# Performance work log

Measured on AMD Instinct MI355X. Metric: run time of the kernel, lower is better.

## Reference

```python
import jax, jax.numpy as jnp
import numpy as np

N_QUBITS = 10
LAYERS = 4


def _ry(theta):
    c = jnp.cos(theta / 2).astype(jnp.complex64)
    s = jnp.sin(theta / 2).astype(jnp.complex64)
    return jnp.array([[c, -s], [s, c]], dtype=jnp.complex64)


def _rot(phi, theta, omega):
    # Rot = RZ(omega) RY(theta) RZ(phi)  (PennyLane convention)
    c = jnp.cos(theta / 2)
    s = jnp.sin(theta / 2)
    e_mm = jnp.exp(-0.5j * (phi + omega))
    e_pm = jnp.exp(0.5j * (phi - omega))
    e_mp = jnp.exp(-0.5j * (phi - omega))
    e_pp = jnp.exp(0.5j * (phi + omega))
    return jnp.array([[e_mm * c, -e_pm * s], [e_mp * s, e_pp * c]], dtype=jnp.complex64)


def _apply_1q(state, U, q):
    # state: (2,)*n complex; contract qubit axis q with 2x2 gate
    s = jnp.tensordot(U, state, axes=[[1], [q]])
    return jnp.moveaxis(s, 0, q)


def _apply_cnot(state, c, t):
    s = jnp.moveaxis(state, (c, t), (0, 1))
    s = jnp.stack([s[0], s[1, ::-1]], axis=0)
    return jnp.moveaxis(s, (0, 1), (c, t))


def _circuit(angles, weights):
    # angles: (n_qubits,) float32, weights: (layers, n_qubits, 3) float32
    n = N_QUBITS
    state = jnp.zeros((2 ** n,), dtype=jnp.complex64).at[0].set(1.0).reshape((2,) * n)
    for q in range(n):  # RY angle embedding
        state = _apply_1q(state, _ry(angles[q]), q)
    for l in range(LAYERS):  # strongly-entangling layers
        for q in range(n):
            state = _apply_1q(state, _rot(weights[l, q, 0], weights[l, q, 1], weights[l, q, 2]), q)
        for q in range(n):  # CNOT ring
            state = _apply_cnot(state, q, (q + 1) % n)
    probs = state.real ** 2 + state.imag ** 2  # (2,)*n
    zexp = []
    for q in range(n):
        p = probs.sum(axis=tuple(a for a in range(n) if a != q))
        zexp.append(p[0] - p[1])
    return jnp.stack(zexp)  # (n_qubits,)


def setup_inputs() -> dict:
    key = jax.random.key(0)
    ks = jax.random.split(key, 6)
    B, D = 8192, 784
    return {
        "x": jax.random.normal(ks[0], (B, D), dtype=jnp.float32),
        "Wp": jax.random.normal(ks[1], (N_QUBITS, D), dtype=jnp.float32) * (1.0 / np.sqrt(D)),
        "bp": jax.random.normal(ks[2], (N_QUBITS,), dtype=jnp.float32) * 0.01,
        "q_weights": jax.random.normal(ks[3], (LAYERS, N_QUBITS, 3), dtype=jnp.float32) * 0.01,
        "Wo": jax.random.normal(ks[4], (10, N_QUBITS), dtype=jnp.float32) * (1.0 / np.sqrt(N_QUBITS)),
        "bo": jax.random.normal(ks[5], (10,), dtype=jnp.float32) * 0.01,
    }


def reference(x, Wp, bp, q_weights, Wo, bo):
    # input projection + tanh
    h = jnp.tanh(x @ Wp.T + bp)  # (B, n_qubits)
    # batched quantum circuit (vmapped statevector simulation)
    q_out = jax.vmap(_circuit, in_axes=(0, None))(h, q_weights)  # (B, n_qubits)
    return q_out @ Wo.T + bo  # (B, 10) logits
```

## Files before the change

kernel.cpp:

```cpp
#include <hip/hip_runtime.h>

#define NQ      10
#define NLAYERS 4
#define D_IN    784
#define BLOCK   256


typedef __attribute__((ext_vector_type(2))) float f2;

__device__ __forceinline__ f2 cswapneg(f2 v) {
    f2 r; r.x = -v.y; r.y = v.x; return r;
}

template<int LB>
__device__ __forceinline__ float lane_xor(float v) {
    if constexpr (LB == 1) {
        return __int_as_float(__builtin_amdgcn_update_dpp(
            0, __float_as_int(v), 0xB1, 0xF, 0xF, false));
    } else if constexpr (LB == 2) {
        return __int_as_float(__builtin_amdgcn_update_dpp(
            0, __float_as_int(v), 0x4E, 0xF, 0xF, false));
    } else {
        return __shfl_xor(v, LB, 64);
    }
}

template<int LB>
__device__ __forceinline__ f2 lane_xor2(f2 v) {
    f2 r; r.x = lane_xor<LB>(v.x); r.y = lane_xor<LB>(v.y); return r;
}

template<int HALF>
__device__ __forceinline__ void plswap(f2 &d, f2 &s) {
    if constexpr (HALF == 32) {
        auto rx = __builtin_amdgcn_permlane32_swap(__float_as_int(d.x), __float_as_int(s.x), false, false);
        auto ry = __builtin_amdgcn_permlane32_swap(__float_as_int(d.y), __float_as_int(s.y), false, false);
        d.x = __int_as_float(rx[0]); s.x = __int_as_float(rx[1]);
        d.y = __int_as_float(ry[0]); s.y = __int_as_float(ry[1]);
    } else {
        auto rx = __builtin_amdgcn_permlane16_swap(__float_as_int(d.x), __float_as_int(s.x), false, false);
        auto ry = __builtin_amdgcn_permlane16_swap(__float_as_int(d.y), __float_as_int(s.y), false, false);
        d.x = __int_as_float(rx[0]); s.x = __int_as_float(rx[1]);
        d.y = __int_as_float(ry[0]); s.y = __int_as_float(ry[1]);
    }
}

template<int HALF>
__device__ __forceinline__ void rot_gate_pl(f2 (&a)[16], float4 gA, float4 gB) {
#pragma unroll
    for (int r = 0; r < 16; r += 2) {
        f2 u = a[r], v = a[r + 1];
        plswap<HALF>(u, v);
        f2 iu = cswapneg(u), iv = cswapneg(v);
        f2 nu = gA.x * u + gA.y * iu + gA.z * v + gA.w * iv;
        f2 nv = gB.x * u + gB.y * iu + gB.z * v + gB.w * iv;
        plswap<HALF>(nu, nv);
        a[r] = nu; a[r + 1] = nv;
    }
}

__device__ __forceinline__ void rot9_fused_pl(f2 (&a)[16], int lane, float4 gA, float4 gB) {
    const bool hi = (lane & 32) != 0;
    const float cux = hi ? gA.z : gA.x, cuy = hi ? gA.w : gA.y;
    const float cvx = hi ? gA.x : gA.z, cvy = hi ? gA.y : gA.w;
    const float dux = hi ? gB.z : gB.x, duy = hi ? gB.w : gB.y;
    const float dvx = hi ? gB.x : gB.z, dvy = hi ? gB.y : gB.w;
#pragma unroll
    for (int r = 0; r < 16; r += 2) {
        f2 u = a[r], v = a[r + 1];
        plswap<32>(u, v);
        f2 iu = cswapneg(u), iv = cswapneg(v);
        f2 nu = cux * u + cuy * iu + cvx * v + cvy * iv;
        f2 nv = dux * u + duy * iu + dvx * v + dvy * iv;
        plswap<32>(nu, nv);
        a[r] = nu; a[r + 1] = nv;
    }
}

template<int P>
__device__ __forceinline__ void rot_gate(f2 (&a)[16], int lane, float4 gA, float4 gB) {
    if constexpr (P >= 4) {
        const int lb = 1 << (P - 4);
        const bool hi = (lane & lb) != 0;
        const float gdx = hi ? gB.z : gA.x, gdy = hi ? gB.w : gA.y;
        const float gox = hi ? gB.x : gA.z, goy = hi ? gB.y : gA.w;
#pragma unroll
        for (int r = 0; r < 16; r++) {
            f2 oa = lane_xor2<lb>(a[r]);
            f2 va = a[r];
            a[r] = gdx * va + gdy * cswapneg(va) + gox * oa + goy * cswapneg(oa);
        }
    } else {
        const int m = 1 << P;
#pragma unroll
        for (int r = 0; r < 16; r++) {
            if (!(r & m)) {
                const int r1 = r | m;
                f2 A0 = a[r], A1 = a[r1];
                f2 ia0 = cswapneg(A0), ia1 = cswapneg(A1);
                a[r]  = gA.x * A0 + gA.y * ia0 + gA.z * A1 + gA.w * ia1;
                a[r1] = gB.x * A0 + gB.y * ia0 + gB.z * A1 + gB.w * ia1;
            }
        }
    }
}

template<int PC, int PT>
__device__ __forceinline__ void cnot_gate(f2 (&a)[16], int lane) {
    if constexpr (PC >= 4 && PT < 4) {
        const int mt = 1 << PT;
        const bool ctl = (lane & (1 << (PC - 4))) != 0;
#pragma unroll
        for (int r = 0; r < 16; r++) {
            if (!(r & mt)) {
                const int r1 = r | mt;
                f2 A0 = a[r], A1 = a[r1];
                f2 n0, n1;
                n0.x = ctl ? A1.x : A0.x;  n0.y = ctl ? A1.y : A0.y;
                n1.x = ctl ? A0.x : A1.x;  n1.y = ctl ? A0.y : A1.y;
                a[r] = n0; a[r1] = n1;
            }
        }
    } else if constexpr (PC < 4 && PT >= 4) {
        const int mc = 1 << PC, mt = 1 << (PT - 4);
#pragma unroll
        for (int r = 0; r < 16; r++) {
            if (r & mc) {
                a[r].x = __shfl_xor(a[r].x, mt, 64);
                a[r].y = __shfl_xor(a[r].y, mt, 64);
            }
        }
    } else {
        const int mc = 1 << PC, mt = 1 << PT;
#pragma unroll
        for (int r = 0; r < 16; r++) {
            if ((r & mc) && !(r & mt)) {
                const int r1 = r | mt;
                f2 t = a[r]; a[r] = a[r1]; a[r1] = t;
            }
        }
    }
}

__global__ __launch_bounds__(BLOCK)
__attribute__((amdgpu_waves_per_eu(4, 8)))
void qnet_kernel(
    const float* __restrict__ x,
    const float* __restrict__ Wp,
    const float* __restrict__ bp,
    const float* __restrict__ qw,
    const float* __restrict__ Wo,
    const float* __restrict__ bo,
    float* __restrict__ out, int B)
{
    __shared__ __align__(16) float gates[NLAYERS * NQ * 8];

    const int tid  = threadIdx.x;
    const int lane = tid & 63;
    const int s    = blockIdx.x * (BLOCK / 64) + (tid >> 6);

    if (tid < NLAYERS * NQ) {
        float phi = qw[tid * 3 + 0];
        float th  = qw[tid * 3 + 1];
        float om  = qw[tid * 3 + 2];
        float sth, cth; sincosf(0.5f * th, &sth, &cth);
        float sap, cap; sincosf(0.5f * (phi + om), &sap, &cap);
        float sam, cam; sincosf(0.5f * (phi - om), &sam, &cam);
        float* g = &gates[tid * 8];
        g[0] =  cap * cth;  g[1] = -sap * cth;
        g[2] = -cam * sth;  g[3] = -sam * sth;
        g[4] =  cam * sth;  g[5] = -sam * sth;
        g[6] =  cap * cth;  g[7] =  sap * cth;
    }
    __syncthreads();
    if (s >= B) return;

    float acc[NQ];
#pragma unroll
    for (int q = 0; q < NQ; q++) acc[q] = 0.f;
    const float* xr = x + (size_t)s * D_IN;
#pragma unroll
    for (int it = 0; it < 3; it++) {
        const int d = (it * 64 + lane) * 4;
        float4 xv = *(const float4*)(xr + d);
#pragma unroll
        for (int q = 0; q < NQ; q++) {
            float4 wv = *(const float4*)(Wp + q * D_IN + d);
            acc[q] += xv.x * wv.x + xv.y * wv.y + xv.z * wv.z + xv.w * wv.w;
        }
    }
    if (lane < 4) {
        const int d = (192 + lane) * 4;
        float4 xv = *(const float4*)(xr + d);
#pragma unroll
        for (int q = 0; q < NQ; q++) {
            float4 wv = *(const float4*)(Wp + q * D_IN + d);
            acc[q] += xv.x * wv.x + xv.y * wv.y + xv.z * wv.z + xv.w * wv.w;
        }
    }
#pragma unroll
    for (int q = 0; q < NQ; q++) {
#pragma unroll
        for (int o = 1; o < 64; o <<= 1) acc[q] += __shfl_xor(acc[q], o, 64);
    }
    float myc = 1.f, mys = 0.f;
    if (lane < NQ) {
        float h = tanhf(acc[lane] + bp[lane]);
        sincosf(0.5f * h, &mys, &myc);
    }

    f2 a[16];
#pragma unroll
    for (int r = 0; r < 16; r++) { a[r].x = 0.f; a[r].y = 0.f; }
    if (lane == 0) a[0].x = 1.f;

    const int bidx = (lane ^ (lane >> 1)) << 2;

    {
        const float* gl = &gates[0];
#define MKMAT(Q) \
        float c0  = __shfl(myc, Q, 64); \
        float ss0 = __shfl(mys, Q, 64); \
        float4 gA = *(const float4*)(gl + Q * 8); \
        float4 gB = *(const float4*)(gl + Q * 8 + 4); \
        float4 Am, Bm; \
        Am.x = gA.x * c0 + gA.z * ss0;  Am.y = gA.y * c0 + gA.w * ss0; \
        Am.z = gA.z * c0 - gA.x * ss0;  Am.w = gA.w * c0 - gA.y * ss0; \
        Bm.x = gB.x * c0 + gB.z * ss0;  Bm.y = gB.y * c0 + gB.w * ss0; \
        Bm.z = gB.z * c0 - gB.x * ss0;  Bm.w = gB.w * c0 - gB.y * ss0;
        { MKMAT(0); rot_gate_pl<32>(a, Am, Bm); }
        { MKMAT(1); rot_gate_pl<16>(a, Am, Bm); }
        { MKMAT(2); rot_gate<7>(a, lane, Am, Bm); }
        { MKMAT(3); rot_gate<6>(a, lane, Am, Bm); }
        { MKMAT(4); rot_gate<5>(a, lane, Am, Bm); }
        { MKMAT(5); rot_gate<4>(a, lane, Am, Bm); }
        { MKMAT(6); rot_gate<3>(a, lane, Am, Bm); }
        { MKMAT(7); rot_gate<2>(a, lane, Am, Bm); }
        { MKMAT(8); rot_gate<1>(a, lane, Am, Bm); }
        { MKMAT(9); rot_gate<0>(a, lane, Am, Bm); }
#undef MKMAT
#pragma unroll
        for (int r = 0; r < 16; r++) {
            a[r].x = __int_as_float(__builtin_amdgcn_ds_bpermute(bidx, __float_as_int(a[r].x)));
            a[r].y = __int_as_float(__builtin_amdgcn_ds_bpermute(bidx, __float_as_int(a[r].y)));
        }
        cnot_gate<4, 3>(a, lane);
        cnot_gate<3, 2>(a, lane);
        cnot_gate<2, 1>(a, lane);
        cnot_gate<1, 0>(a, lane);
    }

    for (int l = 1; l < NLAYERS; l++) {
        const float* gl = &gates[l * NQ * 8];
        {   float4 gA = *(const float4*)(gl);
            float4 gB = *(const float4*)(gl + 4);
            rot9_fused_pl(a, lane, gA, gB); }
        {   float4 gA = *(const float4*)(gl + 8);
            float4 gB = *(const float4*)(gl + 12);
            rot_gate_pl<16>(a, gA, gB); }
#define ROTQ(Q) { float4 gA = *(const float4*)(gl + Q * 8); \
                  float4 gB = *(const float4*)(gl + Q * 8 + 4); \
                  rot_gate<9 - Q>(a, lane, gA, gB); }
        ROTQ(2) ROTQ(3) ROTQ(4)
        ROTQ(5) ROTQ(6) ROTQ(7) ROTQ(8) ROTQ(9)
#undef ROTQ
#pragma unroll
        for (int r = 0; r < 16; r++) {
            a[r].x = __int_as_float(__builtin_amdgcn_ds_bpermute(bidx, __float_as_int(a[r].x)));
            a[r].y = __int_as_float(__builtin_amdgcn_ds_bpermute(bidx, __float_as_int(a[r].y)));
        }
        cnot_gate<4, 3>(a, lane);
        cnot_gate<3, 2>(a, lane);
        cnot_gate<2, 1>(a, lane);
        cnot_gate<1, 0>(a, lane);
    }
    cnot_gate<0, 9>(a, lane);

    float S = 0.f, z3 = 0.f, z2 = 0.f, z1 = 0.f, z0 = 0.f;
#pragma unroll
    for (int r = 0; r < 16; r++) {
        float pa = a[r].x * a[r].x + a[r].y * a[r].y;
        S += pa;
        z3 += (r & 8) ? -pa : pa;
        z2 += (r & 4) ? -pa : pa;
        z1 += (r & 2) ? -pa : pa;
        z0 += (r & 1) ? -pa : pa;
    }
    float zq[NQ];
    zq[6] = z3; zq[7] = z2; zq[8] = z1; zq[9] = z0;
#pragma unroll
    for (int q = 0; q < 6; q++) {
        zq[q] = ((lane >> (5 - q)) & 1) ? -S : S;
    }
#pragma unroll
    for (int q = 0; q < NQ; q++) {
#pragma unroll
        for (int o = 1; o < 64; o <<= 1) {
            zq[q] += __shfl_xor(zq[q], o, 64);
        }
    }

    if (lane < NQ) {
        const float* wrow = Wo + lane * NQ;
        float o0 = bo[lane];
#pragma unroll
        for (int q = 0; q < NQ; q++) o0 += zq[q] * wrow[q];
        out[(size_t)s * NQ + lane] = o0;
    }
}

extern "C" void kernel_launch(void* const* d_in, const int* in_sizes, int n_in,
                              void* d_out, int out_size, void* d_ws, size_t ws_size,
                              hipStream_t stream) {
    const float* x  = (const float*)d_in[0];
    const float* Wp = (const float*)d_in[1];
    const float* bp = (const float*)d_in[2];
    const float* qw = (const float*)d_in[3];
    const float* Wo = (const float*)d_in[4];
    const float* bo = (const float*)d_in[5];
    float* out = (float*)d_out;

    const int B = in_sizes[0] / D_IN;
    const int spb = BLOCK / 64;
    const int blocks = (B + spb - 1) / spb;
    hipLaunchKernelGGL(qnet_kernel, dim3(blocks), dim3(BLOCK), 0, stream,
                       x, Wp, bp, qw, Wo, bo, out, B);
}
```

Baseline: 162.0 us.

## Simulate two samples per wave in split real/imag SoA layout for packed math

Each wave now carries two batch samples, with the state held as separate real and imaginary f2 arrays whose two lanes hold the two samples. This replaces the interleaved complex layout and its cswapneg shuffles, so gate arithmetic can map onto packed FP32 (v_pk_fma) instructions and the cross-lane permutes are shared across two samples. It doubles register usage for the state and halves the number of waves, which may reduce occupancy. It assumes B is even, since s1 is not bounds-checked.

```diff
diff --git a/kernel.cpp b/kernel.cpp
--- a/kernel.cpp
+++ b/kernel.cpp
@@ -8,9 +8,9 @@
 
 typedef __attribute__((ext_vector_type(2))) float f2;
 
-__device__ __forceinline__ f2 cswapneg(f2 v) {
-    f2 r; r.x = -v.y; r.y = v.x; return r;
-}
+__device__ __forceinline__ f2 sp(float v) { f2 r; r.x = v; r.y = v; return r; }
+
+struct G2 { f2 Ax, Ay, Az, Aw, Bx, By, Bz, Bw; };
 
 template<int LB>
 __device__ __forceinline__ float lane_xor(float v) {
@@ -46,49 +46,53 @@
 }
 
 template<int HALF>
-__device__ __forceinline__ void rot_gate_pl(f2 (&a)[16], float4 gA, float4 gB) {
+__device__ __forceinline__ void rot_gate_pl_c(f2 (&re)[16], f2 (&im)[16], const G2& g) {
 #pragma unroll
     for (int r = 0; r < 16; r += 2) {
-        f2 u = a[r], v = a[r + 1];
-        plswap<HALF>(u, v);
-        f2 iu = cswapneg(u), iv = cswapneg(v);
-        f2 nu = gA.x * u + gA.y * iu + gA.z * v + gA.w * iv;
-        f2 nv = gB.x * u + gB.y * iu + gB.z * v + gB.w * iv;
-        plswap<HALF>(nu, nv);
-        a[r] = nu; a[r + 1] = nv;
-    }
-}
-
-__device__ __forceinline__ void rot9_fused_pl(f2 (&a)[16], int lane, float4 gA, float4 gB) {
+        f2 ur = re[r], vr = re[r + 1], ui = im[r], vi = im[r + 1];
+        plswap<HALF>(ur, vr); plswap<HALF>(ui, vi);
+        f2 nur = g.Ax*ur - g.Ay*ui + g.Az*vr - g.Aw*vi;
+        f2 nui = g.Ax*ui + g.Ay*ur + g.Az*vi + g.Aw*vr;
+        f2 nvr = g.Bx*ur - g.By*ui + g.Bz*vr - g.Bw*vi;
+        f2 nvi = g.Bx*ui + g.By*ur + g.Bz*vi + g.Bw*vr;
+        plswap<HALF>(nur, nvr); plswap<HALF>(nui, nvi);
+        re[r] = nur; re[r + 1] = nvr; im[r] = nui; im[r + 1] = nvi;
+    }
+}
+
+__device__ __forceinline__ void rot9_fused_c(f2 (&re)[16], f2 (&im)[16], int lane, const G2& g) {
     const bool hi = (lane & 32) != 0;
-    const float cux = hi ? gA.z : gA.x, cuy = hi ? gA.w : gA.y;
-    const float cvx = hi ? gA.x : gA.z, cvy = hi ? gA.y : gA.w;
-    const float dux = hi ? gB.z : gB.x, duy = hi ? gB.w : gB.y;
-    const float dvx = hi ? gB.x : gB.z, dvy = hi ? gB.y : gB.w;
+    const f2 cAx = hi ? g.Az : g.Ax, cAy = hi ? g.Aw : g.Ay;
+    const f2 cAz = hi ? g.Ax : g.Az, cAw = hi ? g.Ay : g.Aw;
+    const f2 cBx = hi ? g.Bz : g.Bx, cBy = hi ? g.Bw : g.By;
+    const f2 cBz = hi ? g.Bx : g.Bz, cBw = hi ? g.By : g.Bw;
 #pragma unroll
     for (int r = 0; r < 16; r += 2) {
-        f2 u = a[r], v = a[r + 1];
-        plswap<32>(u, v);
-        f2 iu = cswapneg(u), iv = cswapneg(v);
-        f2 nu = cux * u + cuy * iu + cvx * v + cvy * iv;
-        f2 nv = dux * u + duy * iu + dvx * v + dvy * iv;
-        plswap<32>(nu, nv);
-        a[r] = nu; a[r + 1] = nv;
+        f2 ur = re[r], vr = re[r + 1], ui = im[r], vi = im[r + 1];
+        plswap<32>(ur, vr); plswap<32>(ui, vi);
+        f2 nur = cAx*ur - cAy*ui + cAz*vr - cAw*vi;
+        f2 nui = cAx*ui + cAy*ur + cAz*vi + cAw*vr;
+        f2 nvr = cBx*ur - cBy*ui + cBz*vr - cBw*vi;
+        f2 nvi = cBx*ui + cBy*ur + cBz*vi + cBw*vr;
+        plswap<32>(nur, nvr); plswap<32>(nui, nvi);
+        re[r] = nur; re[r + 1] = nvr; im[r] = nui; im[r + 1] = nvi;
     }
 }
 
 template<int P>
-__device__ __forceinline__ void rot_gate(f2 (&a)[16], int lane, float4 gA, float4 gB) {
+__device__ __forceinline__ void rot_gate_c(f2 (&re)[16], f2 (&im)[16], int lane, const G2& g) {
     if constexpr (P >= 4) {
         const int lb = 1 << (P - 4);
         const bool hi = (lane & lb) != 0;
-        const float gdx = hi ? gB.z : gA.x, gdy = hi ? gB.w : gA.y;
-        const float gox = hi ? gB.x : gA.z, goy = hi ? gB.y : gA.w;
-#pragma unroll
-        for (int r = 0; r < 16; r++) {
-            f2 oa = lane_xor2<lb>(a[r]);
-            f2 va = a[r];
-            a[r] = gdx * va + gdy * cswapneg(va) + gox * oa + goy * cswapneg(oa);
+        const f2 gdx = hi ? g.Bz : g.Ax, gdy = hi ? g.Bw : g.Ay;
+        const f2 gox = hi ? g.Bx : g.Az, goy = hi ? g.By : g.Aw;
+#pragma unroll
+        for (int r = 0; r < 16; r++) {
+            f2 ore = lane_xor2<lb>(re[r]);
+            f2 oim = lane_xor2<lb>(im[r]);
+            f2 vr = re[r], vi = im[r];
+            re[r] = gdx*vr - gdy*vi + gox*ore - goy*oim;
+            im[r] = gdx*vi + gdy*vr + gox*oim + goy*ore;
         }
     } else {
         const int m = 1 << P;
@@ -96,17 +100,18 @@
         for (int r = 0; r < 16; r++) {
             if (!(r & m)) {
                 const int r1 = r | m;
-                f2 A0 = a[r], A1 = a[r1];
-                f2 ia0 = cswapneg(A0), ia1 = cswapneg(A1);
-                a[r]  = gA.x * A0 + gA.y * ia0 + gA.z * A1 + gA.w * ia1;
-                a[r1] = gB.x * A0 + gB.y * ia0 + gB.z * A1 + gB.w * ia1;
+                f2 r0r = re[r], r0i = im[r], r1r = re[r1], r1i = im[r1];
+                re[r]  = g.Ax*r0r - g.Ay*r0i + g.Az*r1r - g.Aw*r1i;
+                im[r]  = g.Ax*r0i + g.Ay*r0r + g.Az*r1i + g.Aw*r1r;
+                re[r1] = g.Bx*r0r - g.By*r0i + g.Bz*r1r - g.Bw*r1i;
+                im[r1] = g.Bx*r0i + g.By*r0r + g.Bz*r1i + g.Bw*r1r;
             }
         }
     }
 }
 
 template<int PC, int PT>
-__device__ __forceinline__ void cnot_gate(f2 (&a)[16], int lane) {
+__device__ __forceinline__ void cnot_gate_c(f2 (&re)[16], f2 (&im)[16], int lane) {
     if constexpr (PC >= 4 && PT < 4) {
         const int mt = 1 << PT;
         const bool ctl = (lane & (1 << (PC - 4))) != 0;
@@ -114,11 +119,13 @@
         for (int r = 0; r < 16; r++) {
             if (!(r & mt)) {
                 const int r1 = r | mt;
-                f2 A0 = a[r], A1 = a[r1];
-                f2 n0, n1;
+                f2 A0 = re[r], A1 = re[r1], B0 = im[r], B1 = im[r1];
+                f2 n0, n1, m0, m1;
                 n0.x = ctl ? A1.x : A0.x;  n0.y = ctl ? A1.y : A0.y;
                 n1.x = ctl ? A0.x : A1.x;  n1.y = ctl ? A0.y : A1.y;
-                a[r] = n0; a[r1] = n1;
+                m0.x = ctl ? B1.x : B0.x;  m0.y = ctl ? B1.y : B0.y;
+                m1.x = ctl ? B0.x : B1.x;  m1.y = ctl ? B0.y : B1.y;
+                re[r] = n0; re[r1] = n1; im[r] = m0; im[r1] = m1;
             }
         }
     } else if constexpr (PC < 4 && PT >= 4) {
@@ -126,8 +133,10 @@
 #pragma unroll
         for (int r = 0; r < 16; r++) {
             if (r & mc) {
-                a[r].x = __shfl_xor(a[r].x, mt, 64);
-                a[r].y = __shfl_xor(a[r].y, mt, 64);
+                re[r].x = __shfl_xor(re[r].x, mt, 64);
+                re[r].y = __shfl_xor(re[r].y, mt, 64);
+                im[r].x = __shfl_xor(im[r].x, mt, 64);
+                im[r].y = __shfl_xor(im[r].y, mt, 64);
             }
         }
     } else {
@@ -136,10 +145,20 @@
         for (int r = 0; r < 16; r++) {
             if ((r & mc) && !(r & mt)) {
                 const int r1 = r | mt;
-                f2 t = a[r]; a[r] = a[r1]; a[r1] = t;
+                f2 t = re[r]; re[r] = re[r1]; re[r1] = t;
+                f2 u = im[r]; im[r] = im[r1]; im[r1] = u;
             }
         }
     }
+}
+
+__device__ __forceinline__ G2 load_g(const float* gl, int q) {
+    float4 gA = *(const float4*)(gl + q * 8);
+    float4 gB = *(const float4*)(gl + q * 8 + 4);
+    G2 g;
+    g.Ax = sp(gA.x); g.Ay = sp(gA.y); g.Az = sp(gA.z); g.Aw = sp(gA.w);
+    g.Bx = sp(gB.x); g.By = sp(gB.y); g.Bz = sp(gB.z); g.Bw = sp(gB.w);
+    return g;
 }
 
 __global__ __launch_bounds__(BLOCK)
@@ -157,7 +176,8 @@
 
     const int tid  = threadIdx.x;
     const int lane = tid & 63;
-    const int s    = blockIdx.x * (BLOCK / 64) + (tid >> 6);
+    const int s0   = (blockIdx.x * (BLOCK / 64) + (tid >> 6)) * 2;
+    const int s1   = s0 + 1;
 
     if (tid < NLAYERS * NQ) {
         float phi = qw[tid * 3 + 0];
@@ -173,120 +193,134 @@
         g[6] =  cap * cth;  g[7] =  sap * cth;
     }
     __syncthreads();
-    if (s >= B) return;
-
-    float acc[NQ];
-#pragma unroll
-    for (int q = 0; q < NQ; q++) acc[q] = 0.f;
-    const float* xr = x + (size_t)s * D_IN;
+    if (s0 >= B) return;
+
+    float acc0[NQ], acc1[NQ];
+#pragma unroll
+    for (int q = 0; q < NQ; q++) { acc0[q] = 0.f; acc1[q] = 0.f; }
+    const float* xr0 = x + (size_t)s0 * D_IN;
+    const float* xr1 = x + (size_t)s1 * D_IN;
 #pragma unroll
     for (int it = 0; it < 3; it++) {
         const int d = (it * 64 + lane) * 4;
-        float4 xv = *(const float4*)(xr + d);
+        float4 xv0 = *(const float4*)(xr0 + d);
+        float4 xv1 = *(const float4*)(xr1 + d);
 #pragma unroll
         for (int q = 0; q < NQ; q++) {
             float4 wv = *(const float4*)(Wp + q * D_IN + d);
-            acc[q] += xv.x * wv.x + xv.y * wv.y + xv.z * wv.z + xv.w * wv.w;
+            acc0[q] += xv0.x * wv.x + xv0.y * wv.y + xv0.z * wv.z + xv0.w * wv.w;
+            acc1[q] += xv1.x * wv.x + xv1.y * wv.y + xv1.z * wv.z + xv1.w * wv.w;
         }
     }
     if (lane < 4) {
         const int d = (192 + lane) * 4;
-        float4 xv = *(const float4*)(xr + d);
+        float4 xv0 = *(const float4*)(xr0 + d);
+        float4 xv1 = *(const float4*)(xr1 + d);
 #pragma unroll
         for (int q = 0; q < NQ; q++) {
             float4 wv = *(const float4*)(Wp + q * D_IN + d);
-            acc[q] += xv.x * wv.x + xv.y * wv.y + xv.z * wv.z + xv.w * wv.w;
+            acc0[q] += xv0.x * wv.x + xv0.y * wv.y + xv0.z * wv.z + xv0.w * wv.w;
+            acc1[q] += xv1.x * wv.x + xv1.y * wv.y + xv1.z * wv.z + xv1.w * wv.w;
         }
     }
 #pragma unroll
     for (int q = 0; q < NQ; q++) {
 #pragma unroll
-        for (int o = 1; o < 64; o <<= 1) acc[q] += __shfl_xor(acc[q], o, 64);
-    }
-    float myc = 1.f, mys = 0.f;
+        for (int o = 1; o < 64; o <<= 1) {
+            acc0[q] += __shfl_xor(acc0[q], o, 64);
+            acc1[q] += __shfl_xor(acc1[q], o, 64);
+        }
+    }
+    float myc0 = 1.f, mys0 = 0.f, myc1 = 1.f, mys1 = 0.f;
     if (lane < NQ) {
-        float h = tanhf(acc[lane] + bp[lane]);
-        sincosf(0.5f * h, &mys, &myc);
-    }
-
-    f2 a[16];
-#pragma unroll
-    for (int r = 0; r < 16; r++) { a[r].x = 0.f; a[r].y = 0.f; }
-    if (lane == 0) a[0].x = 1.f;
+        float h0 = tanhf(acc0[lane] + bp[lane]);
+        float h1 = tanhf(acc1[lane] + bp[lane]);
+        sincosf(0.5f * h0, &mys0, &myc0);
+        sincosf(0.5f * h1, &mys1, &myc1);
+    }
+
+    f2 re[16], im[16];
+#pragma unroll
+    for (int r = 0; r < 16; r++) { re[r] = sp(0.f); im[r] = sp(0.f); }
+    if (lane == 0) { re[0].x = 1.f; re[0].y = 1.f; }
 
     const int bidx = (lane ^ (lane >> 1)) << 2;
 
     {
         const float* gl = &gates[0];
-#define MKMAT(Q) \
-        float c0  = __shfl(myc, Q, 64); \
-        float ss0 = __shfl(mys, Q, 64); \
+#define FROTQ(Q, GATECALL) { \
+        f2 cc, ss; \
+        cc.x = __shfl(myc0, Q, 64); cc.y = __shfl(myc1, Q, 64); \
+        ss.x = __shfl(mys0, Q, 64); ss.y = __shfl(mys1, Q, 64); \
         float4 gA = *(const float4*)(gl + Q * 8); \
         float4 gB = *(const float4*)(gl + Q * 8 + 4); \
-        float4 Am, Bm; \
-        Am.x = gA.x * c0 + gA.z * ss0;  Am.y = gA.y * c0 + gA.w * ss0; \
-        Am.z = gA.z * c0 - gA.x * ss0;  Am.w = gA.w * c0 - gA.y * ss0; \
-        Bm.x = gB.x * c0 + gB.z * ss0;  Bm.y = gB.y * c0 + gB.w * ss0; \
-        Bm.z = gB.z * c0 - gB.x * ss0;  Bm.w = gB.w * c0 - gB.y * ss0;
-        { MKMAT(0); rot_gate_pl<32>(a, Am, Bm); }
-        { MKMAT(1); rot_gate_pl<16>(a, Am, Bm); }
-        { MKMAT(2); rot_gate<7>(a, lane, Am, Bm); }
-        { MKMAT(3); rot_gate<6>(a, lane, Am, Bm); }
-        { MKMAT(4); rot_gate<5>(a, lane, Am, Bm); }
-        { MKMAT(5); rot_gate<4>(a, lane, Am, Bm); }
-        { MKMAT(6); rot_gate<3>(a, lane, Am, Bm); }
-        { MKMAT(7); rot_gate<2>(a, lane, Am, Bm); }
-        { MKMAT(8); rot_gate<1>(a, lane, Am, Bm); }
-        { MKMAT(9); rot_gate<0>(a, lane, Am, Bm); }
-#undef MKMAT
-#pragma unroll
-        for (int r = 0; r < 16; r++) {
-            a[r].x = __int_as_float(__builtin_amdgcn_ds_bpermute(bidx, __float_as_int(a[r].x)));
-            a[r].y = __int_as_float(__builtin_amdgcn_ds_bpermute(bidx, __float_as_int(a[r].y)));
-        }
-        cnot_gate<4, 3>(a, lane);
-        cnot_gate<3, 2>(a, lane);
-        cnot_gate<2, 1>(a, lane);
-        cnot_gate<1, 0>(a, lane);
+        G2 g; \
+        g.Ax = gA.x * cc + gA.z * ss;  g.Ay = gA.y * cc + gA.w * ss; \
+        g.Az = gA.z * cc - gA.x * ss;  g.Aw = gA.w * cc - gA.y * ss; \
+        g.Bx = gB.x * cc + gB.z * ss;  g.By = gB.y * cc + gB.w * ss; \
+        g.Bz = gB.z * cc - gB.x * ss;  g.Bw = gB.w * cc - gB.y * ss; \
+        GATECALL; }
+        FROTQ(0, (rot_gate_pl_c<32>(re, im, g)))
+        FROTQ(1, (rot_gate_pl_c<16>(re, im, g)))
+        FROTQ(2, (rot_gate_c<7>(re, im, lane, g)))
+        FROTQ(3, (rot_gate_c<6>(re, im, lane, g)))
+        FROTQ(4, (rot_gate_c<5>(re, im, lane, g)))
+        FROTQ(5, (rot_gate_c<4>(re, im, lane, g)))
+        FROTQ(6, (rot_gate_c<3>(re, im, lane, g)))
+        FROTQ(7, (rot_gate_c<2>(re, im, lane, g)))
+        FROTQ(8, (rot_gate_c<1>(re, im, lane, g)))
+        FROTQ(9, (rot_gate_c<0>(re, im, lane, g)))
+#undef FROTQ
+#pragma unroll
+        for (int r = 0; r < 16; r++) {
+            re[r].x = __int_as_float(__builtin_amdgcn_ds_bpermute(bidx, __float_as_int(re[r].x)));
+            re[r].y = __int_as_float(__builtin_amdgcn_ds_bpermute(bidx, __float_as_int(re[r].y)));
+            im[r].x = __int_as_float(__builtin_amdgcn_ds_bpermute(bidx, __float_as_int(im[r].x)));
+            im[r].y = __int_as_float(__builtin_amdgcn_ds_bpermute(bidx, __float_as_int(im[r].y)));
+        }
+        cnot_gate_c<4, 3>(re, im, lane);
+        cnot_gate_c<3, 2>(re, im, lane);
+        cnot_gate_c<2, 1>(re, im, lane);
+        cnot_gate_c<1, 0>(re, im, lane);
     }
 
     for (int l = 1; l < NLAYERS; l++) {
         const float* gl = &gates[l * NQ * 8];
-        {   float4 gA = *(const float4*)(gl);
-            float4 gB = *(const float4*)(gl + 4);
-            rot9_fused_pl(a, lane, gA, gB); }
-        {   float4 gA = *(const float4*)(gl + 8);
-            float4 gB = *(const float4*)(gl + 12);
-            rot_gate_pl<16>(a, gA, gB); }
-#define ROTQ(Q) { float4 gA = *(const float4*)(gl + Q * 8); \
-                  float4 gB = *(const float4*)(gl + Q * 8 + 4); \
-                  rot_gate<9 - Q>(a, lane, gA, gB); }
-        ROTQ(2) ROTQ(3) ROTQ(4)
-        ROTQ(5) ROTQ(6) ROTQ(7) ROTQ(8) ROTQ(9)
-#undef ROTQ
-#pragma unroll
-        for (int r = 0; r < 16; r++) {
-            a[r].x = __int_as_float(__builtin_amdgcn_ds_bpermute(bidx, __float_as_int(a[r].x)));
-            a[r].y = __int_as_float(__builtin_amdgcn_ds_bpermute(bidx, __float_as_int(a[r].y)));
-        }
-        cnot_gate<4, 3>(a, lane);
-        cnot_gate<3, 2>(a, lane);
-        cnot_gate<2, 1>(a, lane);
-        cnot_gate<1, 0>(a, lane);
-    }
-    cnot_gate<0, 9>(a, lane);
-
-    float S = 0.f, z3 = 0.f, z2 = 0.f, z1 = 0.f, z0 = 0.f;
+        { G2 g = load_g(gl, 0); rot9_fused_c(re, im, lane, g); }
+        { G2 g = load_g(gl, 1); rot_gate_pl_c<16>(re, im, g); }
+        { G2 g = load_g(gl, 2); rot_gate_c<7>(re, im, lane, g); }
+        { G2 g = load_g(gl, 3); rot_gate_c<6>(re, im, lane, g); }
+        { G2 g = load_g(gl, 4); rot_gate_c<5>(re, im, lane, g); }
+        { G2 g = load_g(gl, 5); rot_gate_c<4>(re, im, lane, g); }
+        { G2 g = load_g(gl, 6); rot_gate_c<3>(re, im, lane, g); }
+        { G2 g = load_g(gl, 7); rot_gate_c<2>(re, im, lane, g); }
+        { G2 g = load_g(gl, 8); rot_gate_c<1>(re, im, lane, g); }
+        { G2 g = load_g(gl, 9); rot_gate_c<0>(re, im, lane, g); }
+#pragma unroll
+        for (int r = 0; r < 16; r++) {
+            re[r].x = __int_as_float(__builtin_amdgcn_ds_bpermute(bidx, __float_as_int(re[r].x)));
+            re[r].y = __int_as_float(__builtin_amdgcn_ds_bpermute(bidx, __float_as_int(re[r].y)));
+            im[r].x = __int_as_float(__builtin_amdgcn_ds_bpermute(bidx, __float_as_int(im[r].x)));
+            im[r].y = __int_as_float(__builtin_amdgcn_ds_bpermute(bidx, __float_as_int(im[r].y)));
+        }
+        cnot_gate_c<4, 3>(re, im, lane);
+        cnot_gate_c<3, 2>(re, im, lane);
+        cnot_gate_c<2, 1>(re, im, lane);
+        cnot_gate_c<1, 0>(re, im, lane);
+    }
+    cnot_gate_c<0, 9>(re, im, lane);
+
+    f2 S = sp(0.f), z3 = sp(0.f), z2 = sp(0.f), z1 = sp(0.f), z0 = sp(0.f);
 #pragma unroll
     for (int r = 0; r < 16; r++) {
-        float pa = a[r].x * a[r].x + a[r].y * a[r].y;
+        f2 pa = re[r] * re[r] + im[r] * im[r];
         S += pa;
-        z3 += (r & 8) ? -pa : pa;
-        z2 += (r & 4) ? -pa : pa;
-        z1 += (r & 2) ? -pa : pa;
-        z0 += (r & 1) ? -pa : pa;
-    }
-    float zq[NQ];
+        if (r & 8) z3 -= pa; else z3 += pa;
+        if (r & 4) z2 -= pa; else z2 += pa;
+        if (r & 2) z1 -= pa; else z1 += pa;
+        if (r & 1) z0 -= pa; else z0 += pa;
+    }
+    f2 zq[NQ];
     zq[6] = z3; zq[7] = z2; zq[8] = z1; zq[9] = z0;
 #pragma unroll
     for (int q = 0; q < 6; q++) {
@@ -296,16 +330,22 @@
     for (int q = 0; q < NQ; q++) {
 #pragma unroll
         for (int o = 1; o < 64; o <<= 1) {
-            zq[q] += __shfl_xor(zq[q], o, 64);
+            zq[q].x += __shfl_xor(zq[q].x, o, 64);
+            zq[q].y += __shfl_xor(zq[q].y, o, 64);
         }
     }
 
     if (lane < NQ) {
         const float* wrow = Wo + lane * NQ;
-        float o0 = bo[lane];
-#pragma unroll
-        for (int q = 0; q < NQ; q++) o0 += zq[q] * wrow[q];
-        out[(size_t)s * NQ + lane] = o0;
+        float o0 = bo[lane], o1 = o0;
+#pragma unroll
+        for (int q = 0; q < NQ; q++) {
+            float w = wrow[q];
+            o0 += zq[q].x * w;
+            o1 += zq[q].y * w;
+        }
+        out[(size_t)s0 * NQ + lane] = o0;
+        out[(size_t)s1 * NQ + lane] = o1;
     }
 }
 
@@ -321,8 +361,9 @@
     float* out = (float*)d_out;
 
     const int B = in_sizes[0] / D_IN;
+    const int waves = (B + 1) / 2;
     const int spb = BLOCK / 64;
-    const int blocks = (B + spb - 1) / spb;
+    const int blocks = (waves + spb - 1) / spb;
     hipLaunchKernelGGL(qnet_kernel, dim3(blocks), dim3(BLOCK), 0, stream,
                        x, Wp, bp, qw, Wo, bo, out, B);
 }
```

Result: faster. 149.3 us (-7.8%).

## Split statevector into real/imag planes with packed pair layout and fused CNOT ring

Applied to the files above, without the earlier changes.

Reorganizes the per-lane statevector from 16 interleaved complex values into separate real and imaginary f2 arrays, so the gate arithmetic can use packed two-wide FP32 math without swap-and-negate shuffles. Qubit 9 becomes an intra-f2 component mapping and is handled by a dedicated rot_comp. The CNOT ring is folded into fixed register swaps and component swaps. It also adds a DPP row-mirror path for lane-xor 8 and relaxes waves_per_eu to allow more registers. Risks are correctness of the remapped qubit indices and higher register pressure lowering occupancy.

```diff
diff --git a/kernel.cpp b/kernel.cpp
--- a/kernel.cpp
+++ b/kernel.cpp
@@ -5,29 +5,29 @@
 #define D_IN    784
 #define BLOCK   256
 
-
 typedef __attribute__((ext_vector_type(2))) float f2;
 
-__device__ __forceinline__ f2 cswapneg(f2 v) {
-    f2 r; r.x = -v.y; r.y = v.x; return r;
-}
+__device__ __forceinline__ f2 swapc(f2 v) { return __builtin_shufflevector(v, v, 1, 0); }
 
 template<int LB>
-__device__ __forceinline__ float lane_xor(float v) {
+__device__ __forceinline__ float lx(float v) {
     if constexpr (LB == 1) {
         return __int_as_float(__builtin_amdgcn_update_dpp(
             0, __float_as_int(v), 0xB1, 0xF, 0xF, false));
     } else if constexpr (LB == 2) {
         return __int_as_float(__builtin_amdgcn_update_dpp(
             0, __float_as_int(v), 0x4E, 0xF, 0xF, false));
+    } else if constexpr (LB == 8) {
+        return __int_as_float(__builtin_amdgcn_update_dpp(
+            0, __float_as_int(v), 0x128, 0xF, 0xF, false));
     } else {
         return __shfl_xor(v, LB, 64);
     }
 }
 
 template<int LB>
-__device__ __forceinline__ f2 lane_xor2(f2 v) {
-    f2 r; r.x = lane_xor<LB>(v.x); r.y = lane_xor<LB>(v.y); return r;
+__device__ __forceinline__ f2 lx2(f2 v) {
+    f2 r; r.x = lx<LB>(v.x); r.y = lx<LB>(v.y); return r;
 }
 
 template<int HALF>
@@ -46,104 +46,111 @@
 }
 
 template<int HALF>
-__device__ __forceinline__ void rot_gate_pl(f2 (&a)[16], float4 gA, float4 gB) {
-#pragma unroll
-    for (int r = 0; r < 16; r += 2) {
-        f2 u = a[r], v = a[r + 1];
-        plswap<HALF>(u, v);
-        f2 iu = cswapneg(u), iv = cswapneg(v);
-        f2 nu = gA.x * u + gA.y * iu + gA.z * v + gA.w * iv;
-        f2 nv = gB.x * u + gB.y * iu + gB.z * v + gB.w * iv;
-        plswap<HALF>(nu, nv);
-        a[r] = nu; a[r + 1] = nv;
-    }
-}
-
-__device__ __forceinline__ void rot9_fused_pl(f2 (&a)[16], int lane, float4 gA, float4 gB) {
-    const bool hi = (lane & 32) != 0;
-    const float cux = hi ? gA.z : gA.x, cuy = hi ? gA.w : gA.y;
-    const float cvx = hi ? gA.x : gA.z, cvy = hi ? gA.y : gA.w;
-    const float dux = hi ? gB.z : gB.x, duy = hi ? gB.w : gB.y;
-    const float dvx = hi ? gB.x : gB.z, dvy = hi ? gB.y : gB.w;
-#pragma unroll
-    for (int r = 0; r < 16; r += 2) {
-        f2 u = a[r], v = a[r + 1];
-        plswap<32>(u, v);
-        f2 iu = cswapneg(u), iv = cswapneg(v);
-        f2 nu = cux * u + cuy * iu + cvx * v + cvy * iv;
-        f2 nv = dux * u + duy * iu + dvx * v + dvy * iv;
-        plswap<32>(nu, nv);
-        a[r] = nu; a[r + 1] = nv;
-    }
-}
-
-template<int P>
-__device__ __forceinline__ void rot_gate(f2 (&a)[16], int lane, float4 gA, float4 gB) {
-    if constexpr (P >= 4) {
-        const int lb = 1 << (P - 4);
-        const bool hi = (lane & lb) != 0;
-        const float gdx = hi ? gB.z : gA.x, gdy = hi ? gB.w : gA.y;
-        const float gox = hi ? gB.x : gA.z, goy = hi ? gB.y : gA.w;
-#pragma unroll
-        for (int r = 0; r < 16; r++) {
-            f2 oa = lane_xor2<lb>(a[r]);
-            f2 va = a[r];
-            a[r] = gdx * va + gdy * cswapneg(va) + gox * oa + goy * cswapneg(oa);
+__device__ __forceinline__ void rot_pl(f2 (&re)[8], f2 (&im)[8], float4 A, float4 B) {
+#pragma unroll
+    for (int a = 0; a < 8; a += 2) {
+        f2 ur = re[a], vr = re[a + 1], ui = im[a], vi = im[a + 1];
+        plswap<HALF>(ur, vr); plswap<HALF>(ui, vi);
+        f2 nur = A.x*ur - A.y*ui + A.z*vr - A.w*vi;
+        f2 nui = A.x*ui + A.y*ur + A.z*vi + A.w*vr;
+        f2 nvr = B.x*ur - B.y*ui + B.z*vr - B.w*vi;
+        f2 nvi = B.x*ui + B.y*ur + B.z*vi + B.w*vr;
+        plswap<HALF>(nur, nvr); plswap<HALF>(nui, nvi);
+        re[a] = nur; re[a + 1] = nvr; im[a] = nui; im[a + 1] = nvi;
+    }
+}
+
+__device__ __forceinline__ void rot0_fused(f2 (&re)[8], f2 (&im)[8], float4 A, float4 B) {
+    f2 CuAr, CuAi, CvAr, CvAi, CuBr, CuBi, CvBr, CvBi;
+    CuAr.x = A.x; CuAr.y = A.z;   CuAi.x = A.y; CuAi.y = A.w;
+    CvAr.x = A.z; CvAr.y = A.x;   CvAi.x = A.w; CvAi.y = A.y;
+    CuBr.x = B.x; CuBr.y = B.z;   CuBi.x = B.y; CuBi.y = B.w;
+    CvBr.x = B.z; CvBr.y = B.x;   CvBi.x = B.w; CvBi.y = B.y;
+#pragma unroll
+    for (int a = 0; a < 8; a += 2) {
+        f2 ur = re[a], vr = re[a + 1], ui = im[a], vi = im[a + 1];
+        plswap<32>(ur, vr); plswap<32>(ui, vi);
+        f2 nur = CuAr*ur - CuAi*ui + CvAr*vr - CvAi*vi;
+        f2 nui = CuAr*ui + CuAi*ur + CvAr*vi + CvAi*vr;
+        f2 nvr = CuBr*ur - CuBi*ui + CvBr*vr - CvBi*vi;
+        f2 nvi = CuBr*ui + CuBi*ur + CvBr*vi + CvBi*vr;
+        plswap<32>(nur, nvr); plswap<32>(nui, nvi);
+        re[a] = nur; re[a + 1] = nvr; im[a] = nui; im[a + 1] = nvi;
+    }
+}
+
+template<int LB>
+__device__ __forceinline__ void rot_lane(f2 (&re)[8], f2 (&im)[8], int lane, float4 A, float4 B) {
+    const bool hi = (lane & LB) != 0;
+    const float gdx = hi ? B.z : A.x, gdy = hi ? B.w : A.y;
+    const float gox = hi ? B.x : A.z, goy = hi ? B.y : A.w;
+#pragma unroll
+    for (int a = 0; a < 8; a++) {
+        f2 ore = lx2<LB>(re[a]);
+        f2 oim = lx2<LB>(im[a]);
+        f2 vr = re[a], vi = im[a];
+        re[a] = gdx*vr - gdy*vi + gox*ore - goy*oim;
+        im[a] = gdx*vi + gdy*vr + gox*oim + goy*ore;
+    }
+}
+
+template<int MB>
+__device__ __forceinline__ void rot_reg(f2 (&re)[8], f2 (&im)[8], float4 A, float4 B) {
+#pragma unroll
+    for (int a = 0; a < 8; a++) {
+        if (!(a & MB)) {
+            const int a1 = a | MB;
+            f2 r0r = re[a], r0i = im[a], r1r = re[a1], r1i = im[a1];
+            re[a]  = A.x*r0r - A.y*r0i + A.z*r1r - A.w*r1i;
+            im[a]  = A.x*r0i + A.y*r0r + A.z*r1i + A.w*r1r;
+            re[a1] = B.x*r0r - B.y*r0i + B.z*r1r - B.w*r1i;
+            im[a1] = B.x*r0i + B.y*r0r + B.z*r1i + B.w*r1r;
         }
-    } else {
-        const int m = 1 << P;
-#pragma unroll
-        for (int r = 0; r < 16; r++) {
-            if (!(r & m)) {
-                const int r1 = r | m;
-                f2 A0 = a[r], A1 = a[r1];
-                f2 ia0 = cswapneg(A0), ia1 = cswapneg(A1);
-                a[r]  = gA.x * A0 + gA.y * ia0 + gA.z * A1 + gA.w * ia1;
-                a[r1] = gB.x * A0 + gB.y * ia0 + gB.z * A1 + gB.w * ia1;
-            }
-        }
-    }
-}
-
-template<int PC, int PT>
-__device__ __forceinline__ void cnot_gate(f2 (&a)[16], int lane) {
-    if constexpr (PC >= 4 && PT < 4) {
-        const int mt = 1 << PT;
-        const bool ctl = (lane & (1 << (PC - 4))) != 0;
-#pragma unroll
-        for (int r = 0; r < 16; r++) {
-            if (!(r & mt)) {
-                const int r1 = r | mt;
-                f2 A0 = a[r], A1 = a[r1];
-                f2 n0, n1;
-                n0.x = ctl ? A1.x : A0.x;  n0.y = ctl ? A1.y : A0.y;
-                n1.x = ctl ? A0.x : A1.x;  n1.y = ctl ? A0.y : A1.y;
-                a[r] = n0; a[r1] = n1;
-            }
-        }
-    } else if constexpr (PC < 4 && PT >= 4) {
-        const int mc = 1 << PC, mt = 1 << (PT - 4);
-#pragma unroll
-        for (int r = 0; r < 16; r++) {
-            if (r & mc) {
-                a[r].x = __shfl_xor(a[r].x, mt, 64);
-                a[r].y = __shfl_xor(a[r].y, mt, 64);
-            }
-        }
-    } else {
-        const int mc = 1 << PC, mt = 1 << PT;
-#pragma unroll
-        for (int r = 0; r < 16; r++) {
-            if ((r & mc) && !(r & mt)) {
-                const int r1 = r | mt;
-                f2 t = a[r]; a[r] = a[r1]; a[r1] = t;
-            }
-        }
-    }
+    }
+}
+
+__device__ __forceinline__ void rot_comp(f2 (&re)[8], f2 (&im)[8], float4 A, float4 B) {
+    f2 K1, K2, K3, K4;
+    K1.x = A.x; K1.y = B.z;   K2.x = -A.y; K2.y = -B.w;
+    K3.x = A.z; K3.y = B.x;   K4.x = -A.w; K4.y = -B.y;
+#pragma unroll
+    for (int a = 0; a < 8; a++) {
+        f2 sre = swapc(re[a]), sim = swapc(im[a]);
+        f2 nre = K1*re[a] + K2*im[a] + K3*sre + K4*sim;
+        f2 nim = K1*im[a] - K2*re[a] + K3*sim - K4*sre;
+        re[a] = nre; im[a] = nim;
+    }
+}
+
+__device__ __forceinline__ void swapf2(f2 &a, f2 &b) { f2 t = a; a = b; b = t; }
+
+__device__ __forceinline__ void ring(f2 (&re)[8], f2 (&im)[8], int lane, int bidx) {
+#pragma unroll
+    for (int a = 0; a < 8; a++) {
+        re[a].x = __int_as_float(__builtin_amdgcn_ds_bpermute(bidx, __float_as_int(re[a].x)));
+        re[a].y = __int_as_float(__builtin_amdgcn_ds_bpermute(bidx, __float_as_int(re[a].y)));
+        im[a].x = __int_as_float(__builtin_amdgcn_ds_bpermute(bidx, __float_as_int(im[a].x)));
+        im[a].y = __int_as_float(__builtin_amdgcn_ds_bpermute(bidx, __float_as_int(im[a].y)));
+    }
+    const bool ctl = (lane & 1) != 0;
+#pragma unroll
+    for (int a = 0; a < 4; a++) {
+        f2 A0 = re[a], A1 = re[a + 4], B0 = im[a], B1 = im[a + 4];
+        f2 n0, n1, m0, m1;
+        n0.x = ctl ? A1.x : A0.x;  n0.y = ctl ? A1.y : A0.y;
+        n1.x = ctl ? A0.x : A1.x;  n1.y = ctl ? A0.y : A1.y;
+        m0.x = ctl ? B1.x : B0.x;  m0.y = ctl ? B1.y : B0.y;
+        m1.x = ctl ? B0.x : B1.x;  m1.y = ctl ? B0.y : B1.y;
+        re[a] = n0; re[a + 4] = n1; im[a] = m0; im[a + 4] = m1;
+    }
+    swapf2(re[4], re[6]); swapf2(re[5], re[7]); swapf2(im[4], im[6]); swapf2(im[5], im[7]);
+    swapf2(re[2], re[3]); swapf2(re[6], re[7]); swapf2(im[2], im[3]); swapf2(im[6], im[7]);
+#pragma unroll
+    for (int a = 1; a < 8; a += 2) { re[a] = swapc(re[a]); im[a] = swapc(im[a]); }
 }
 
 __global__ __launch_bounds__(BLOCK)
-__attribute__((amdgpu_waves_per_eu(4, 8)))
+__attribute__((amdgpu_waves_per_eu(2, 8)))
 void qnet_kernel(
     const float* __restrict__ x,
     const float* __restrict__ Wp,
@@ -209,95 +216,81 @@
         sincosf(0.5f * h, &mys, &myc);
     }
 
-    f2 a[16];
-#pragma unroll
-    for (int r = 0; r < 16; r++) { a[r].x = 0.f; a[r].y = 0.f; }
-    if (lane == 0) a[0].x = 1.f;
+    f2 re[8], im[8];
+#pragma unroll
+    for (int a = 0; a < 8; a++) { re[a].x = 0.f; re[a].y = 0.f; im[a].x = 0.f; im[a].y = 0.f; }
+    if (lane == 0) re[0].x = 1.f;
 
     const int bidx = (lane ^ (lane >> 1)) << 2;
 
     {
         const float* gl = &gates[0];
 #define MKMAT(Q) \
-        float c0  = __shfl(myc, Q, 64); \
-        float ss0 = __shfl(mys, Q, 64); \
+        float c0 = __shfl(myc, Q, 64), s0 = __shfl(mys, Q, 64); \
         float4 gA = *(const float4*)(gl + Q * 8); \
         float4 gB = *(const float4*)(gl + Q * 8 + 4); \
         float4 Am, Bm; \
-        Am.x = gA.x * c0 + gA.z * ss0;  Am.y = gA.y * c0 + gA.w * ss0; \
-        Am.z = gA.z * c0 - gA.x * ss0;  Am.w = gA.w * c0 - gA.y * ss0; \
-        Bm.x = gB.x * c0 + gB.z * ss0;  Bm.y = gB.y * c0 + gB.w * ss0; \
-        Bm.z = gB.z * c0 - gB.x * ss0;  Bm.w = gB.w * c0 - gB.y * ss0;
-        { MKMAT(0); rot_gate_pl<32>(a, Am, Bm); }
-        { MKMAT(1); rot_gate_pl<16>(a, Am, Bm); }
-        { MKMAT(2); rot_gate<7>(a, lane, Am, Bm); }
-        { MKMAT(3); rot_gate<6>(a, lane, Am, Bm); }
-        { MKMAT(4); rot_gate<5>(a, lane, Am, Bm); }
-        { MKMAT(5); rot_gate<4>(a, lane, Am, Bm); }
-        { MKMAT(6); rot_gate<3>(a, lane, Am, Bm); }
-        { MKMAT(7); rot_gate<2>(a, lane, Am, Bm); }
-        { MKMAT(8); rot_gate<1>(a, lane, Am, Bm); }
-        { MKMAT(9); rot_gate<0>(a, lane, Am, Bm); }
+        Am.x = gA.x * c0 + gA.z * s0;  Am.y = gA.y * c0 + gA.w * s0; \
+        Am.z = gA.z * c0 - gA.x * s0;  Am.w = gA.w * c0 - gA.y * s0; \
+        Bm.x = gB.x * c0 + gB.z * s0;  Bm.y = gB.y * c0 + gB.w * s0; \
+        Bm.z = gB.z * c0 - gB.x * s0;  Bm.w = gB.w * c0 - gB.y * s0;
+        { MKMAT(0); rot_pl<32>(re, im, Am, Bm); }
+        { MKMAT(1); rot_pl<16>(re, im, Am, Bm); }
+        { MKMAT(2); rot_lane<8>(re, im, lane, Am, Bm); }
+        { MKMAT(3); rot_lane<4>(re, im, lane, Am, Bm); }
+        { MKMAT(4); rot_lane<2>(re, im, lane, Am, Bm); }
+        { MKMAT(5); rot_lane<1>(re, im, lane, Am, Bm); }
+        { MKMAT(6); rot_reg<4>(re, im, Am, Bm); }
+        { MKMAT(7); rot_reg<2>(re, im, Am, Bm); }
+        { MKMAT(8); rot_reg<1>(re, im, Am, Bm); }
+        { MKMAT(9); rot_comp(re, im, Am, Bm); }
 #undef MKMAT
-#pragma unroll
-        for (int r = 0; r < 16; r++) {
-            a[r].x = __int_as_float(__builtin_amdgcn_ds_bpermute(bidx, __float_as_int(a[r].x)));
-            a[r].y = __int_as_float(__builtin_amdgcn_ds_bpermute(bidx, __float_as_int(a[r].y)));
-        }
-        cnot_gate<4, 3>(a, lane);
-        cnot_gate<3, 2>(a, lane);
-        cnot_gate<2, 1>(a, lane);
-        cnot_gate<1, 0>(a, lane);
+        ring(re, im, lane, bidx);
     }
 
     for (int l = 1; l < NLAYERS; l++) {
         const float* gl = &gates[l * NQ * 8];
-        {   float4 gA = *(const float4*)(gl);
-            float4 gB = *(const float4*)(gl + 4);
-            rot9_fused_pl(a, lane, gA, gB); }
-        {   float4 gA = *(const float4*)(gl + 8);
-            float4 gB = *(const float4*)(gl + 12);
-            rot_gate_pl<16>(a, gA, gB); }
-#define ROTQ(Q) { float4 gA = *(const float4*)(gl + Q * 8); \
-                  float4 gB = *(const float4*)(gl + Q * 8 + 4); \
-                  rot_gate<9 - Q>(a, lane, gA, gB); }
-        ROTQ(2) ROTQ(3) ROTQ(4)
-        ROTQ(5) ROTQ(6) ROTQ(7) ROTQ(8) ROTQ(9)
-#undef ROTQ
-#pragma unroll
-        for (int r = 0; r < 16; r++) {
-            a[r].x = __int_as_float(__builtin_amdgcn_ds_bpermute(bidx, __float_as_int(a[r].x)));
-            a[r].y = __int_as_float(__builtin_amdgcn_ds_bpermute(bidx, __float_as_int(a[r].y)));
-        }
-        cnot_gate<4, 3>(a, lane);
-        cnot_gate<3, 2>(a, lane);
-        cnot_gate<2, 1>(a, lane);
-        cnot_gate<1, 0>(a, lane);
-    }
-    cnot_gate<0, 9>(a, lane);
-
-    float S = 0.f, z3 = 0.f, z2 = 0.f, z1 = 0.f, z0 = 0.f;
-#pragma unroll
-    for (int r = 0; r < 16; r++) {
-        float pa = a[r].x * a[r].x + a[r].y * a[r].y;
-        S += pa;
-        z3 += (r & 8) ? -pa : pa;
-        z2 += (r & 4) ? -pa : pa;
-        z1 += (r & 2) ? -pa : pa;
-        z0 += (r & 1) ? -pa : pa;
-    }
+#define GMAT(Q) *(const float4*)(gl + Q * 8), *(const float4*)(gl + Q * 8 + 4)
+        rot0_fused(re, im, GMAT(0));
+        rot_pl<16>(re, im, GMAT(1));
+        rot_lane<8>(re, im, lane, GMAT(2));
+        rot_lane<4>(re, im, lane, GMAT(3));
+        rot_lane<2>(re, im, lane, GMAT(4));
+        rot_lane<1>(re, im, lane, GMAT(5));
+        rot_reg<4>(re, im, GMAT(6));
+        rot_reg<2>(re, im, GMAT(7));
+        rot_reg<1>(re, im, GMAT(8));
+        rot_comp(re, im, GMAT(9));
+#undef GMAT
+        ring(re, im, lane, bidx);
+    }
+
+    f2 S2 = {0.f, 0.f}, z62 = {0.f, 0.f}, z72 = {0.f, 0.f}, z82 = {0.f, 0.f};
+#pragma unroll
+    for (int a = 0; a < 8; a++) {
+        f2 p = re[a] * re[a] + im[a] * im[a];
+        S2 += p;
+        if (a & 4) z62 -= p; else z62 += p;
+        if (a & 2) z72 -= p; else z72 += p;
+        if (a & 1) z82 -= p; else z82 += p;
+    }
+    const float Ssum = S2.x + S2.y;
+    const float Sdif = S2.x - S2.y;
     float zq[NQ];
-    zq[6] = z3; zq[7] = z2; zq[8] = z1; zq[9] = z0;
-#pragma unroll
-    for (int q = 0; q < 6; q++) {
-        zq[q] = ((lane >> (5 - q)) & 1) ? -S : S;
-    }
+    zq[0] = (lane & 32) ? -Sdif : Sdif;
+    zq[1] = (lane & 16) ? -Ssum : Ssum;
+    zq[2] = (lane &  8) ? -Ssum : Ssum;
+    zq[3] = (lane &  4) ? -Ssum : Ssum;
+    zq[4] = (lane &  2) ? -Ssum : Ssum;
+    zq[5] = (lane &  1) ? -Ssum : Ssum;
+    zq[6] = z62.x + z62.y;
+    zq[7] = z72.x + z72.y;
+    zq[8] = z82.x + z82.y;
+    zq[9] = Sdif;
 #pragma unroll
     for (int q = 0; q < NQ; q++) {
 #pragma unroll
-        for (int o = 1; o < 64; o <<= 1) {
-            zq[q] += __shfl_xor(zq[q], o, 64);
-        }
+        for (int o = 1; o < 64; o <<= 1) zq[q] += __shfl_xor(zq[q], o, 64);
     }
 
     if (lane < NQ) {
```

New measurement: 147.2 us. 1.1x faster.
